# Optimization experiments

Hardware: AMD Instinct MI355X
Metric: run time of the kernel (lower is better)

## Reference

```python
import jax, jax.numpy as jnp
import numpy as np

HIDDEN = 2048
NUM_HEADS = 16
NUM_KV_HEADS = 4
HEAD_DIM = HIDDEN // NUM_HEADS  # 128
ROPE_THETA = 1000000.0
B, S = 2, 2048


def setup_inputs() -> dict:
    key = jax.random.key(0)
    ks = jax.random.split(key, 10)
    sc = 0.02
    return {
        "hidden_states": jax.random.normal(ks[0], (B, S, HIDDEN), jnp.float32),
        "position_ids": jnp.broadcast_to(jnp.arange(S, dtype=jnp.int32), (B, S)),
        "Wq": jax.random.normal(ks[1], (HIDDEN, NUM_HEADS * HEAD_DIM), jnp.float32) * sc,
        "bq": jnp.zeros((NUM_HEADS * HEAD_DIM,), jnp.float32),
        "Wk": jax.random.normal(ks[2], (HIDDEN, NUM_KV_HEADS * HEAD_DIM), jnp.float32) * sc,
        "bk": jnp.zeros((NUM_KV_HEADS * HEAD_DIM,), jnp.float32),
        "Wv": jax.random.normal(ks[3], (HIDDEN, NUM_KV_HEADS * HEAD_DIM), jnp.float32) * sc,
        "bv": jnp.zeros((NUM_KV_HEADS * HEAD_DIM,), jnp.float32),
        "Wo": jax.random.normal(ks[4], (NUM_HEADS * HEAD_DIM, HIDDEN), jnp.float32) * sc,
        "bo": jnp.zeros((HIDDEN,), jnp.float32),
    }


def _rope_cos_sin(position_ids, dtype):
    # inv_freq: [head_dim/2]
    inv_freq = 1.0 / (ROPE_THETA ** (jnp.arange(0, HEAD_DIM, 2, dtype=jnp.float32) / HEAD_DIM))
    freqs = position_ids.astype(jnp.float32)[:, :, None] * inv_freq[None, None, :]  # [B,S,d/2]
    emb = jnp.concatenate([freqs, freqs], axis=-1)  # [B,S,d]
    return jnp.cos(emb).astype(dtype), jnp.sin(emb).astype(dtype)


def _rotate_half(x):
    h = x.shape[-1] // 2
    return jnp.concatenate([-x[..., h:], x[..., :h]], axis=-1)


def _attention(hidden_states, position_ids, Wq, bq, Wk, bk, Wv, bv, Wo, bo):
    bsz, q_len, _ = hidden_states.shape
    q = (hidden_states @ Wq + bq).reshape(bsz, q_len, NUM_HEADS, HEAD_DIM).transpose(0, 2, 1, 3)
    k = (hidden_states @ Wk + bk).reshape(bsz, q_len, NUM_KV_HEADS, HEAD_DIM).transpose(0, 2, 1, 3)
    v = (hidden_states @ Wv + bv).reshape(bsz, q_len, NUM_KV_HEADS, HEAD_DIM).transpose(0, 2, 1, 3)

    cos, sin = _rope_cos_sin(position_ids, hidden_states.dtype)
    cos = cos[:, None, :, :]  # [B,1,S,d]
    sin = sin[:, None, :, :]
    q = q * cos + _rotate_half(q) * sin
    k = k * cos + _rotate_half(k) * sin

    # repeat_kv (GQA): [B,kvh,S,d] -> [B,H,S,d]
    n_rep = NUM_HEADS // NUM_KV_HEADS
    k = jnp.repeat(k, n_rep, axis=1)
    v = jnp.repeat(v, n_rep, axis=1)

    scale = 1.0 / jnp.sqrt(jnp.array(HEAD_DIM, hidden_states.dtype))
    scores = jnp.einsum('bhqd,bhkd->bhqk', q, k) * scale  # [B,H,S,S]
    causal = jnp.tril(jnp.ones((q_len, q_len), bool))
    scores = jnp.where(causal[None, None], scores, jnp.finfo(scores.dtype).min)
    probs = jax.nn.softmax(scores.astype(jnp.float32), axis=-1).astype(hidden_states.dtype)
    attn = jnp.einsum('bhqk,bhkd->bhqd', probs, v)
    attn = attn.transpose(0, 2, 1, 3).reshape(bsz, q_len, HIDDEN)
    return attn @ Wo + bo


def reference(hidden_states, position_ids, Wq, bq, Wk, bk, Wv, bv, Wo, bo):
    return _attention(hidden_states, position_ids, Wq, bq, Wk, bk, Wv, bv, Wo, bo)
```

## Files before the change

kernel.cpp:

```cpp
#include <hip/hip_runtime.h>
#include <cmath>

#define HIDDEN 2048
#define NH 16
#define NKV 4
#define HD 128
#define SEQ 2048
#define BATCH 2

typedef unsigned short ushort_t;
typedef short bf16x8 __attribute__((ext_vector_type(8)));
typedef float f32x4 __attribute__((ext_vector_type(4)));
typedef ushort_t u16x4 __attribute__((ext_vector_type(4)));

__device__ __forceinline__ ushort_t f2bf(float f) {
    union { float f; unsigned int u; } v; v.f = f;
    unsigned int r = v.u + 0x7fffu + ((v.u >> 16) & 1u);
    return (ushort_t)(r >> 16);
}
__device__ __forceinline__ ushort_t f2bf_trunc(float f) {
    union { float f; unsigned int u; } v; v.f = f;
    return (ushort_t)(v.u >> 16);
}

__device__ __forceinline__ f32x4 mfma16(bf16x8 a, bf16x8 b, f32x4 c) {
    return __builtin_amdgcn_mfma_f32_16x16x32_bf16(a, b, c, 0, 0, 0);
}

__device__ __forceinline__ void load_lds16(const void* g, void* l) {
    __builtin_amdgcn_global_load_lds((const __attribute__((address_space(1))) unsigned int*)g,
                                     (__attribute__((address_space(3))) unsigned int*)l,
                                     16, 0, 0);
}


__global__ __launch_bounds__(256) void convert_x(const float* __restrict__ x,
                                                 ushort_t* __restrict__ xb, int n4) {
    int g = blockIdx.x * 256 + threadIdx.x;
    if (g >= n4) return;
    float4 v = ((const float4*)x)[g];
    u16x4 o;
    o[0] = f2bf(v.x); o[1] = f2bf(v.y); o[2] = f2bf(v.z); o[3] = f2bf(v.w);
    ((u16x4*)xb)[g] = o;
}

__global__ __launch_bounds__(256) void transpose_all(const float* __restrict__ Wq,
                                                     const float* __restrict__ Wk,
                                                     const float* __restrict__ Wv,
                                                     const float* __restrict__ Wo,
                                                     ushort_t* __restrict__ WqkvT,
                                                     ushort_t* __restrict__ WoT) {
    const int z = blockIdx.z;
    const float* W;
    ushort_t* WT;
    int N;
    if (z == 0)      { W = Wq; WT = WqkvT;                        N = 2048; }
    else if (z == 1) { W = Wk; WT = WqkvT + 2048ull * 2048;       N = 512;  }
    else if (z == 2) { W = Wv; WT = WqkvT + 2560ull * 2048;       N = 512;  }
    else             { W = Wo; WT = WoT;                          N = 2048; }
    const int K = 2048;
    const int n0 = blockIdx.x * 64, k0 = blockIdx.y * 64;
    if (n0 >= N) return;
    __shared__ ushort_t T[64][72];
    const int t = threadIdx.x;
    for (int idx = t; idx < 64 * 16; idx += 256) {
        int r = idx >> 4, c4 = (idx & 15) << 2;
        float4 v = *(const float4*)&W[(size_t)(k0 + r) * N + n0 + c4];
        T[r][c4 + 0] = f2bf(v.x); T[r][c4 + 1] = f2bf(v.y);
        T[r][c4 + 2] = f2bf(v.z); T[r][c4 + 3] = f2bf(v.w);
    }
    __syncthreads();
    for (int idx = t; idx < 64 * 16; idx += 256) {
        int n = idx >> 4, kg = (idx & 15) << 2;
        u16x4 o;
        o[0] = T[kg + 0][n]; o[1] = T[kg + 1][n];
        o[2] = T[kg + 2][n]; o[3] = T[kg + 3][n];
        *(u16x4*)&WT[(size_t)(n0 + n) * K + k0 + kg] = o;
    }
}

template <int MODE, int BK>
__global__ __launch_bounds__(256) void gemm_bt(const ushort_t* __restrict__ A,
                                               const ushort_t* __restrict__ Bt,
                                               const float* __restrict__ bias,
                                               const float* __restrict__ bias2,
                                               const float* __restrict__ bias3,
                                               void* __restrict__ out,
                                               void* __restrict__ out2,
                                               void* __restrict__ out3,
                                               int M, int N, int K,
                                               const int* __restrict__ posids) {
    constexpr int CH = BK / 32;
    __shared__ __align__(16) ushort_t As[2 * CH * 4096];
    __shared__ __align__(16) ushort_t Bs[2 * CH * 4096];
    const int tid = threadIdx.x;
    const int w = tid >> 6, lane = tid & 63, quad = lane >> 4, l16 = lane & 15;
    const int m0 = blockIdx.y * 128, n0 = blockIdx.x * 128;

    f32x4 acc[2][8];
    for (int i = 0; i < 2; i++)
        for (int j = 0; j < 8; j++)
            for (int e = 0; e < 4; e++) acc[i][j][e] = 0.0f;

    const int rr = lane >> 2;
    const int gc8 = (((lane & 3) ^ ((lane >> 3) & 3)) << 3);
    const ushort_t* Ag = A + (size_t)(m0 + w * 32 + rr) * K + gc8;
    const ushort_t* Bg = Bt + (size_t)(n0 + w * 32 + rr) * K + gc8;
    ushort_t* Asw = As + w * 1024;
    ushort_t* Bsw = Bs + w * 1024;

    auto stage = [&](int bi, int k0) {
#pragma unroll
        for (int kc = 0; kc < CH; kc++) {
            const ushort_t* ag = Ag + k0 + kc * 32;
            const ushort_t* bg = Bg + k0 + kc * 32;
            ushort_t* la = Asw + (bi * CH + kc) * 4096;
            ushort_t* lb = Bsw + (bi * CH + kc) * 4096;
            load_lds16(ag, la);
            load_lds16(ag + (size_t)16 * K, la + 512);
            load_lds16(bg, lb);
            load_lds16(bg + (size_t)16 * K, lb + 512);
        }
    };

    const int nk = K / BK;
    const int rsw = ((l16 >> 1) & 3);
    stage(0, 0);
    __syncthreads();

    for (int ki = 0; ki < nk; ki++) {
        const int cur = ki & 1;
        if (ki + 1 < nk) stage(cur ^ 1, (ki + 1) * BK);
#pragma unroll
        for (int kc = 0; kc < CH; kc++) {
            const ushort_t* Ab = &As[(cur * CH + kc) * 4096];
            const ushort_t* Bb = &Bs[(cur * CH + kc) * 4096];
            bf16x8 af[2];
#pragma unroll
            for (int i = 0; i < 2; i++)
                af[i] = *(const bf16x8*)&Ab[(w * 32 + i * 16 + l16) * 32 + (quad ^ rsw) * 8];
#pragma unroll
            for (int j = 0; j < 8; j++) {
                bf16x8 bf = *(const bf16x8*)&Bb[(j * 16 + l16) * 32 + (quad ^ rsw) * 8];
#pragma unroll
                for (int i = 0; i < 2; i++) acc[i][j] = mfma16(af[i], bf, acc[i][j]);
            }
        }
        __syncthreads();
    }

    if (MODE == 0) {
        float* O = (float*)out;
#pragma unroll
        for (int i = 0; i < 2; i++)
#pragma unroll
            for (int r = 0; r < 4; r++) {
                int row = m0 + w * 32 + i * 16 + quad * 4 + r;
#pragma unroll
                for (int j = 0; j < 8; j++) {
                    int col = n0 + j * 16 + l16;
                    O[(size_t)row * N + col] = acc[i][j][r] + bias[col];
                }
            }
    } else {
        if (n0 < 2048) {
            ushort_t* O = (ushort_t*)out;
            const int h = n0 >> 7;
            const float scale = 0.08838834764831845f;
#pragma unroll
            for (int i = 0; i < 2; i++)
#pragma unroll
                for (int r = 0; r < 4; r++) {
                    int row = m0 + w * 32 + i * 16 + quad * 4 + r;
                    int b = row >> 11, s = row & (SEQ - 1);
                    float pos = (float)posids[row];
                    size_t obase = ((size_t)(b * NH + h) * SEQ + s) * HD;
#pragma unroll
                    for (int j = 0; j < 4; j++) {
                        int dl = j * 16 + l16;
                        float x1 = acc[i][j][r] + bias[n0 + dl];
                        float x2 = acc[i][j + 4][r] + bias[n0 + dl + 64];
                        float ang = pos * __expf(-0.21586735246819178f * (float)dl);
                        float sn, cs;
                        __sincosf(ang, &sn, &cs);
                        O[obase + dl]      = f2bf((x1 * cs - x2 * sn) * scale);
                        O[obase + dl + 64] = f2bf((x2 * cs + x1 * sn) * scale);
                    }
                }
        } else if (n0 < 2560) {
            ushort_t* O = (ushort_t*)out2;
            const int n0k = n0 - 2048;
            const int h = n0k >> 7;
#pragma unroll
            for (int i = 0; i < 2; i++)
#pragma unroll
                for (int r = 0; r < 4; r++) {
                    int row = m0 + w * 32 + i * 16 + quad * 4 + r;
                    int b = row >> 11, s = row & (SEQ - 1);
                    float pos = (float)posids[row];
                    size_t obase = ((size_t)(b * NKV + h) * SEQ + s) * HD;
#pragma unroll
                    for (int j = 0; j < 4; j++) {
                        int dl = j * 16 + l16;
                        float x1 = acc[i][j][r] + bias2[n0k + dl];
                        float x2 = acc[i][j + 4][r] + bias2[n0k + dl + 64];
                        float ang = pos * __expf(-0.21586735246819178f * (float)dl);
                        float sn, cs;
                        __sincosf(ang, &sn, &cs);
                        O[obase + dl]      = f2bf(x1 * cs - x2 * sn);
                        O[obase + dl + 64] = f2bf(x2 * cs + x1 * sn);
                    }
                }
        } else {
            ushort_t* O = (ushort_t*)out3;
            const int n0v = n0 - 2560;
            const int h = n0v >> 7;
#pragma unroll
            for (int i = 0; i < 2; i++)
#pragma unroll
                for (int r = 0; r < 4; r++) {
                    int row = m0 + w * 32 + i * 16 + quad * 4 + r;
                    int b = row >> 11, s = row & (SEQ - 1);
#pragma unroll
                    for (int j = 0; j < 8; j++) {
                        int d = j * 16 + l16;
                        float v = acc[i][j][r] + bias3[n0v + d];
                        O[((size_t)(b * NKV + h) * HD + d) * SEQ + s] = f2bf(v);
                    }
                }
        }
    }
}

__global__ __launch_bounds__(256) void flash(const ushort_t* __restrict__ Qr,
                                             const ushort_t* __restrict__ Kr,
                                             const ushort_t* __restrict__ Vt,
                                             ushort_t* __restrict__ Attn) {
    __shared__ __align__(16) ushort_t Ksh[2 * 4 * 64 * 32];
    __shared__ __align__(16) ushort_t Vsh[2 * 2 * 128 * 32];
    __shared__ __align__(16) ushort_t Ps[4 * 16 * 72];
    const int tid = threadIdx.x;
    const int w = tid >> 6, lane = tid & 63, quad = lane >> 4, l16 = lane & 15;
    const int x = blockIdx.x, h = blockIdx.y, b = blockIdx.z;
    const int qt = b ? x : (gridDim.x - 1 - x);
    const int q0 = qt * 128;
    const int nkt = 2 * qt + 2;
    const int hkv = h >> 2;
    const ushort_t* Kg = Kr + ((size_t)(b * NKV + hkv) * SEQ) * HD;
    const ushort_t* Vg = Vt + ((size_t)(b * NKV + hkv) * HD) * SEQ;

    const int p = lane >> 2;
    const int gc8 = (((lane & 3) ^ ((lane >> 3) & 3)) << 3);
    const ushort_t* kst = Kg + (size_t)p * HD + w * 32 + gc8;
    const ushort_t* vst = Vg + (size_t)((w & 1) * 64 + p) * SEQ + (w >> 1) * 32 + gc8;
    ushort_t* ksl = Ksh + w * 2048;
    ushort_t* vsl = Vsh + (w >> 1) * 4096 + (w & 1) * 2048;

    auto stage = [&](int bi, int kv0) {
        const ushort_t* gk = kst + (size_t)kv0 * HD;
        ushort_t* lk = ksl + bi * 8192;
        load_lds16(gk, lk);
        load_lds16(gk + (size_t)16 * HD, lk + 512);
        load_lds16(gk + (size_t)32 * HD, lk + 1024);
        load_lds16(gk + (size_t)48 * HD, lk + 1536);
        const ushort_t* gv = vst + kv0;
        ushort_t* lv = vsl + bi * 8192;
        load_lds16(gv, lv);
        load_lds16(gv + (size_t)16 * SEQ, lv + 512);
        load_lds16(gv + (size_t)32 * SEQ, lv + 1024);
        load_lds16(gv + (size_t)48 * SEQ, lv + 1536);
    };

    bf16x8 aq[2][4];
#pragma unroll
    for (int st = 0; st < 2; st++) {
        const size_t qrow = ((size_t)(b * NH + h) * SEQ + q0 + st * 64 + w * 16 + l16) * HD;
#pragma unroll
        for (int kc = 0; kc < 4; kc++)
            aq[st][kc] = *(const bf16x8*)&Qr[qrow + kc * 32 + quad * 8];
    }

    f32x4 o[2][8];
#pragma unroll
    for (int st = 0; st < 2; st++)
#pragma unroll
        for (int j = 0; j < 8; j++)
#pragma unroll
            for (int e = 0; e < 4; e++) o[st][j][e] = 0.0f;
    f32x4 ls2[2];
#pragma unroll
    for (int st = 0; st < 2; st++)
        for (int e = 0; e < 4; e++) ls2[st][e] = 0.0f;
    bf16x8 ones;
#pragma unroll
    for (int e = 0; e < 8; e++) ones[e] = (short)0x3F80;

    ushort_t* Pw = &Ps[w * 16 * 72];
    const int rsw8 = ((l16 >> 1) & 3) << 3;

    stage(0, 0);
    __syncthreads();

    for (int kt = 0; kt < nkt; kt++) {
        const int kv0 = kt * 64;
        const int cur = kt & 1;
        if (kt + 1 < nkt) stage(cur ^ 1, kv0 + 64);

        const ushort_t* Kb = Ksh + cur * 8192;
        const ushort_t* Vb = Vsh + cur * 8192;

#pragma unroll
        for (int st = 0; st < 2; st++) {
            if (st == 0 && kt == 2 * qt + 1) continue;

            f32x4 sa[4];
#pragma unroll
            for (int nt = 0; nt < 4; nt++)
#pragma unroll
                for (int e = 0; e < 4; e++) sa[nt][e] = 0.0f;
#pragma unroll
            for (int kc = 0; kc < 4; kc++) {
#pragma unroll
                for (int nt = 0; nt < 4; nt++) {
                    bf16x8 bk = *(const bf16x8*)&Kb[kc * 2048 + nt * 512 + l16 * 32 +
                                                    ((quad * 8) ^ rsw8)];
                    sa[nt] = mfma16(aq[st][kc], bk, sa[nt]);
                }
            }

            if ((kt >> 1) == qt && (kt & 1) == st) {
#pragma unroll
                for (int nt = 0; nt < 4; nt++)
#pragma unroll
                    for (int r = 0; r < 4; r++) {
                        int kvg = kv0 + nt * 16 + l16;
                        int qg = q0 + st * 64 + w * 16 + quad * 4 + r;
                        if (kvg > qg) sa[nt][r] = -1e30f;
                    }
            }

#pragma unroll
            for (int nt = 0; nt < 4; nt++)
#pragma unroll
                for (int r = 0; r < 4; r++)
                    Pw[(quad * 4 + r) * 72 + nt * 16 + l16] = f2bf_trunc(__expf(sa[nt][r]));

#pragma unroll
            for (int kc = 0; kc < 2; kc++) {
                bf16x8 ap = *(const bf16x8*)&Pw[l16 * 72 + kc * 32 + quad * 8];
                ls2[st] = mfma16(ap, ones, ls2[st]);
#pragma unroll
                for (int j = 0; j < 8; j++) {
                    bf16x8 bv = *(const bf16x8*)&Vb[kc * 4096 + (j * 16 + l16) * 32 +
                                                    ((quad * 8) ^ rsw8)];
                    o[st][j] = mfma16(ap, bv, o[st][j]);
                }
            }
        }
        __syncthreads();
    }

#pragma unroll
    for (int st = 0; st < 2; st++)
#pragma unroll
        for (int r = 0; r < 4; r++) {
            float inv = 1.0f / ls2[st][r];
            int row = b * SEQ + q0 + st * 64 + w * 16 + quad * 4 + r;
            size_t obase = (size_t)row * HIDDEN + h * HD;
#pragma unroll
            for (int j = 0; j < 8; j++) Attn[obase + j * 16 + l16] = f2bf(o[st][j][r] * inv);
        }
}

extern "C" void kernel_launch(void* const* d_in, const int* in_sizes, int n_in,
                              void* d_out, int out_size, void* d_ws, size_t ws_size,
                              hipStream_t stream) {
    const float* hs = (const float*)d_in[0];
    const int* posids = (const int*)d_in[1];
    const float* Wq = (const float*)d_in[2];
    const float* bq = (const float*)d_in[3];
    const float* Wk = (const float*)d_in[4];
    const float* bk = (const float*)d_in[5];
    const float* Wv = (const float*)d_in[6];
    const float* bv = (const float*)d_in[7];
    const float* Wo = (const float*)d_in[8];
    const float* bo = (const float*)d_in[9];
    float* out = (float*)d_out;

    char* ws = (char*)d_ws;
    size_t off = 0;
    auto alloc = [&](size_t bytes) {
        char* p = ws + off;
        off += (bytes + 255) & ~(size_t)255;
        return p;
    };
    ushort_t* Xb     = (ushort_t*)alloc(4096ull * 2048 * 2);
    ushort_t* WqkvT  = (ushort_t*)alloc(3072ull * 2048 * 2);
    ushort_t* WoT    = (ushort_t*)alloc(2048ull * 2048 * 2);
    ushort_t* Qr     = (ushort_t*)alloc((size_t)BATCH * NH * SEQ * HD * 2);
    ushort_t* Kr     = (ushort_t*)alloc((size_t)BATCH * NKV * SEQ * HD * 2);
    ushort_t* Vtr    = (ushort_t*)alloc((size_t)BATCH * NKV * HD * SEQ * 2);
    ushort_t* Attn   = (ushort_t*)alloc(4096ull * 2048 * 2);

    convert_x<<<4096 * 2048 / 4 / 256, 256, 0, stream>>>(hs, Xb, 4096 * 2048 / 4);
    transpose_all<<<dim3(32, 32, 4), 256, 0, stream>>>(Wq, Wk, Wv, Wo, WqkvT, WoT);

    gemm_bt<2, 32><<<dim3(24, 32), 256, 0, stream>>>(Xb, WqkvT, bq, bk, bv,
                                                     Qr, Kr, Vtr, 4096, 3072, 2048, posids);

    flash<<<dim3(SEQ / 128, NH, BATCH), 256, 0, stream>>>(Qr, Kr, Vtr, Attn);

    gemm_bt<0, 64><<<dim3(16, 32), 256, 0, stream>>>(Attn, WoT, bo, nullptr, nullptr,
                                                     out, nullptr, nullptr, 4096, 2048, 2048, nullptr);
}
```

Before: 348.2 us.

## Triple-buffer GEMM LDS staging with partial vmcnt waits before barriers

Replaces the double-buffered GEMM mainloop with a three-stage ring of 32-wide K tiles. Loads are issued two tiles ahead, and a custom barrier waits only until at most four outstanding global-to-LDS loads remain, so the next tile's loads keep flowing while the current tile is computed. This targets load latency that was exposed by the full drain at each __syncthreads. The output GEMM now also uses BK=32 instead of 64, which means more barriers per K. Correctness relies on the hand-written vmcnt counting matching the four loads issued per stage.

Measured after the change: 355.5 us. 2.1% more time.

```diff
diff --git a/kernel.cpp b/kernel.cpp
--- a/kernel.cpp
+++ b/kernel.cpp
@@ -31,6 +31,13 @@
     __builtin_amdgcn_global_load_lds((const __attribute__((address_space(1))) unsigned int*)g,
                                      (__attribute__((address_space(3))) unsigned int*)l,
                                      16, 0, 0);
+}
+
+__device__ __forceinline__ void barrier_keep4() {
+    asm volatile("s_waitcnt vmcnt(4)\n\ts_barrier" ::: "memory");
+}
+__device__ __forceinline__ void barrier_drain() {
+    asm volatile("s_waitcnt vmcnt(0)\n\ts_barrier" ::: "memory");
 }
 
 
@@ -79,7 +86,7 @@
     }
 }
 
-template <int MODE, int BK>
+template <int MODE>
 __global__ __launch_bounds__(256) void gemm_bt(const ushort_t* __restrict__ A,
                                                const ushort_t* __restrict__ Bt,
                                                const float* __restrict__ bias,
@@ -90,9 +97,8 @@
                                                void* __restrict__ out3,
                                                int M, int N, int K,
                                                const int* __restrict__ posids) {
-    constexpr int CH = BK / 32;
-    __shared__ __align__(16) ushort_t As[2 * CH * 4096];
-    __shared__ __align__(16) ushort_t Bs[2 * CH * 4096];
+    __shared__ __align__(16) ushort_t As[3 * 4096];
+    __shared__ __align__(16) ushort_t Bs[3 * 4096];
     const int tid = threadIdx.x;
     const int w = tid >> 6, lane = tid & 63, quad = lane >> 4, l16 = lane & 15;
     const int m0 = blockIdx.y * 128, n0 = blockIdx.x * 128;
@@ -110,44 +116,49 @@
     ushort_t* Bsw = Bs + w * 1024;
 
     auto stage = [&](int bi, int k0) {
-#pragma unroll
-        for (int kc = 0; kc < CH; kc++) {
-            const ushort_t* ag = Ag + k0 + kc * 32;
-            const ushort_t* bg = Bg + k0 + kc * 32;
-            ushort_t* la = Asw + (bi * CH + kc) * 4096;
-            ushort_t* lb = Bsw + (bi * CH + kc) * 4096;
-            load_lds16(ag, la);
-            load_lds16(ag + (size_t)16 * K, la + 512);
-            load_lds16(bg, lb);
-            load_lds16(bg + (size_t)16 * K, lb + 512);
+        const ushort_t* ag = Ag + k0;
+        const ushort_t* bg = Bg + k0;
+        ushort_t* la = Asw + bi * 4096;
+        ushort_t* lb = Bsw + bi * 4096;
+        load_lds16(ag, la);
+        load_lds16(ag + (size_t)16 * K, la + 512);
+        load_lds16(bg, lb);
+        load_lds16(bg + (size_t)16 * K, lb + 512);
+    };
+
+    const int rsw = ((l16 >> 1) & 3);
+    auto compute = [&](int bi) {
+        const ushort_t* Ab = &As[bi * 4096];
+        const ushort_t* Bb = &Bs[bi * 4096];
+        bf16x8 af[2];
+#pragma unroll
+        for (int i = 0; i < 2; i++)
+            af[i] = *(const bf16x8*)&Ab[(w * 32 + i * 16 + l16) * 32 + (quad ^ rsw) * 8];
+#pragma unroll
+        for (int j = 0; j < 8; j++) {
+            bf16x8 bf = *(const bf16x8*)&Bb[(j * 16 + l16) * 32 + (quad ^ rsw) * 8];
+#pragma unroll
+            for (int i = 0; i < 2; i++) acc[i][j] = mfma16(af[i], bf, acc[i][j]);
         }
     };
 
-    const int nk = K / BK;
-    const int rsw = ((l16 >> 1) & 3);
+    const int nk = K >> 5;
     stage(0, 0);
-    __syncthreads();
-
-    for (int ki = 0; ki < nk; ki++) {
-        const int cur = ki & 1;
-        if (ki + 1 < nk) stage(cur ^ 1, (ki + 1) * BK);
-#pragma unroll
-        for (int kc = 0; kc < CH; kc++) {
-            const ushort_t* Ab = &As[(cur * CH + kc) * 4096];
-            const ushort_t* Bb = &Bs[(cur * CH + kc) * 4096];
-            bf16x8 af[2];
-#pragma unroll
-            for (int i = 0; i < 2; i++)
-                af[i] = *(const bf16x8*)&Ab[(w * 32 + i * 16 + l16) * 32 + (quad ^ rsw) * 8];
-#pragma unroll
-            for (int j = 0; j < 8; j++) {
-                bf16x8 bf = *(const bf16x8*)&Bb[(j * 16 + l16) * 32 + (quad ^ rsw) * 8];
-#pragma unroll
-                for (int i = 0; i < 2; i++) acc[i][j] = mfma16(af[i], bf, acc[i][j]);
-            }
-        }
-        __syncthreads();
-    }
+    stage(1, 32);
+    barrier_keep4();
+
+    int cb = 0, sb = 2;
+    for (int ki = 0; ki < nk - 2; ki++) {
+        stage(sb, (ki + 2) << 5);
+        compute(cb);
+        barrier_keep4();
+        cb = (cb == 2) ? 0 : cb + 1;
+        sb = (sb == 2) ? 0 : sb + 1;
+    }
+    compute(cb);
+    cb = (cb == 2) ? 0 : cb + 1;
+    barrier_drain();
+    compute(cb);
 
     if (MODE == 0) {
         float* O = (float*)out;
@@ -405,11 +416,11 @@
     convert_x<<<4096 * 2048 / 4 / 256, 256, 0, stream>>>(hs, Xb, 4096 * 2048 / 4);
     transpose_all<<<dim3(32, 32, 4), 256, 0, stream>>>(Wq, Wk, Wv, Wo, WqkvT, WoT);
 
-    gemm_bt<2, 32><<<dim3(24, 32), 256, 0, stream>>>(Xb, WqkvT, bq, bk, bv,
-                                                     Qr, Kr, Vtr, 4096, 3072, 2048, posids);
+    gemm_bt<2><<<dim3(24, 32), 256, 0, stream>>>(Xb, WqkvT, bq, bk, bv,
+                                                 Qr, Kr, Vtr, 4096, 3072, 2048, posids);
 
     flash<<<dim3(SEQ / 128, NH, BATCH), 256, 0, stream>>>(Qr, Kr, Vtr, Attn);
 
-    gemm_bt<0, 64><<<dim3(16, 32), 256, 0, stream>>>(Attn, WoT, bo, nullptr, nullptr,
-                                                     out, nullptr, nullptr, 4096, 2048, 2048, nullptr);
-}
+    gemm_bt<0><<<dim3(16, 32), 256, 0, stream>>>(Attn, WoT, bo, nullptr, nullptr,
+                                                 out, nullptr, nullptr, 4096, 2048, 2048, nullptr);
+}
```
